# Kernel optimization log

Measured on AMD Instinct MI355X. Metric: run time of the kernel, lower is better.

The kernel has to match this reference:

```python
import jax, jax.numpy as jnp
import numpy as np

B, N, D, H = 32, 64, 128, 256
LN_EPS = 1e-5


def _mlp(x, W1, b1, g, beta, W2, b2):
    # Linear -> LayerNorm -> GELU (exact erf) -> Linear
    h = x @ W1 + b1
    mu = jnp.mean(h, axis=-1, keepdims=True)
    var = jnp.var(h, axis=-1, keepdims=True)
    h = (h - mu) * jax.lax.rsqrt(var + LN_EPS) * g + beta
    h = jax.nn.gelu(h, approximate=False)
    return h @ W2 + b2


def setup_inputs() -> dict:
    key = jax.random.key(0)
    ks = jax.random.split(key, 10)
    s = lambda fan_in: 1.0 / np.sqrt(fan_in)
    return {
        "slots": jax.random.normal(ks[0], (B, N, D), dtype=jnp.float32),
        "adjacency": jax.random.uniform(ks[1], (B, N, N), dtype=jnp.float32),
        # edge_net params
        "We1": jax.random.uniform(ks[2], (2 * D, H), minval=-s(2 * D), maxval=s(2 * D), dtype=jnp.float32),
        "be1": jnp.zeros((H,), jnp.float32),
        "ge": jnp.ones((H,), jnp.float32),
        "bge": jnp.zeros((H,), jnp.float32),
        "We2": jax.random.uniform(ks[3], (H, D), minval=-s(H), maxval=s(H), dtype=jnp.float32),
        "be2": jnp.zeros((D,), jnp.float32),
        # node_net params
        "Wn1": jax.random.uniform(ks[4], (2 * D, H), minval=-s(2 * D), maxval=s(2 * D), dtype=jnp.float32),
        "bn1": jnp.zeros((H,), jnp.float32),
        "gn": jnp.ones((H,), jnp.float32),
        "bgn": jnp.zeros((H,), jnp.float32),
        "Wn2": jax.random.uniform(ks[5], (H, D), minval=-s(H), maxval=s(H), dtype=jnp.float32),
        "bn2": jnp.zeros((D,), jnp.float32),
    }


def reference(slots, adjacency, We1, be1, ge, bge, We2, be2, Wn1, bn1, gn, bgn, Wn2, bn2):
    b, n, d = slots.shape
    # all-pairs edge features: receiver i, sender j -> [B,N,N,2D]
    ei = jnp.broadcast_to(slots[:, :, None, :], (b, n, n, d))
    ej = jnp.broadcast_to(slots[:, None, :, :], (b, n, n, d))
    edge_feat = jnp.concatenate([ei, ej], axis=-1)
    edge_out = _mlp(edge_feat, We1, be1, ge, bge, We2, be2)  # [B,N,N,D]
    # mask diagonal (i != j) and weight by adjacency, then reduce over j
    mask = 1.0 - jnp.eye(n, dtype=slots.dtype)
    w = adjacency * mask  # [B,N,N]
    messages = jnp.einsum('bij,bijd->bid', w, edge_out)
    node_input = jnp.concatenate([slots, messages], axis=-1)
    delta = _mlp(node_input, Wn1, bn1, gn, bgn, Wn2, bn2)
    return slots + delta
```

## Files before the change

kernel.cpp:

```cpp
#include <hip/hip_runtime.h>

#define NB 32
#define NN 64
#define ND 128
#define NH 256
#define LN_EPS 1e-5f
#define RP 4

__device__ __forceinline__ float gelu2(float x) {
    const float au  = fabsf(x);
    const float xpa = x + au;
    const float z   = au * 0.70710678118654752440f;
    const float z2  = z * z;
    const float pc  = fmaf(0.078108f, z, 0.000972f);
    const float pb  = fmaf(0.278393f, z, 1.0f);
    const float p   = fmaf(z2, fmaf(z, pc, 0.230389f), pb);
    const float p2  = p * p;
    const float r   = __builtin_amdgcn_rcpf(p2 * p2);
    return fmaf(-au, r, xpa);
}
__device__ __forceinline__ float gelu_h(float x) { return 0.5f * gelu2(x); }

__global__ __launch_bounds__(256) void k_pre(const float* __restrict__ slots,
                                             const float* __restrict__ We1,
                                             const float* __restrict__ be1,
                                             const float* __restrict__ Wn1,
                                             const float* __restrict__ We2,
                                             const float* __restrict__ be2,
                                             float* __restrict__ Pt,
                                             float* __restrict__ Qm,
                                             float* __restrict__ XW,
                                             float4* __restrict__ rowstats,
                                             float* __restrict__ WC,
                                             float* __restrict__ v) {
    __shared__ float xs[RP][ND];
    __shared__ float red[4][RP][4];
    const int t = threadIdx.x;

    if (blockIdx.x >= 512) {
        const int bid2 = blockIdx.x - 512;
        if (bid2 == 64) {
            __shared__ float bs[ND];
            if (t < ND) bs[t] = be2[t];
            __syncthreads();
            float acc = 0.f;
            #pragma unroll 4
            for (int d = 0; d < ND; ++d) acc = fmaf(bs[d], Wn1[(ND + d) * NH + t], acc);
            v[t] = acc;
            return;
        }
        const int k0 = bid2 * 4;
        __shared__ float ws[4][ND];
        #pragma unroll
        for (int i = 0; i < 2; ++i) {
            const int idx = t + i * 256;
            ws[idx >> 7][idx & 127] = We2[(k0 + (idx >> 7)) * ND + (idx & 127)];
        }
        __syncthreads();
        float acc[4] = {0.f, 0.f, 0.f, 0.f};
        #pragma unroll 4
        for (int d = 0; d < ND; ++d) {
            const float wn = Wn1[(ND + d) * NH + t];
            #pragma unroll
            for (int r = 0; r < 4; ++r) acc[r] = fmaf(ws[r][d], wn, acc[r]);
        }
        #pragma unroll
        for (int r = 0; r < 4; ++r) WC[(k0 + r) * NH + t] = acc[r];
        return;
    }

    const int r0 = blockIdx.x * RP;
    const int lane = t & 63, wave = t >> 6;
    #pragma unroll
    for (int i = 0; i < 2; ++i) {
        const int idx = t + i * 256;
        xs[idx >> 7][idx & 127] = slots[(size_t)(r0 + (idx >> 7)) * ND + (idx & 127)];
    }
    __syncthreads();
    float pt[RP], qq[RP], xw[RP];
    const float bb = be1[t];
    #pragma unroll
    for (int r = 0; r < RP; ++r) { pt[r] = bb; qq[r] = 0.f; xw[r] = 0.f; }
    #pragma unroll 4
    for (int d = 0; d < ND; ++d) {
        const float wt  = We1[d * NH + t];
        const float wbt = We1[(ND + d) * NH + t];
        const float wn  = Wn1[d * NH + t];
        #pragma unroll
        for (int r = 0; r < RP; ++r) {
            const float x = xs[r][d];
            pt[r] = fmaf(x, wt,  pt[r]);
            qq[r] = fmaf(x, wbt, qq[r]);
            xw[r] = fmaf(x, wn,  xw[r]);
        }
    }
    #pragma unroll
    for (int r = 0; r < RP; ++r) {
        const size_t row = (size_t)(r0 + r);
        Pt[row * NH + t] = pt[r];
        Qm[row * NH + t] = qq[r];
        XW[row * NH + t] = xw[r];
    }
    float s1[RP], s2[RP], s3[RP], s4[RP];
    #pragma unroll
    for (int r = 0; r < RP; ++r) {
        s1[r] = pt[r]; s2[r] = pt[r] * pt[r];
        s3[r] = qq[r]; s4[r] = qq[r] * qq[r];
    }
    #pragma unroll
    for (int off = 32; off; off >>= 1) {
        #pragma unroll
        for (int r = 0; r < RP; ++r) {
            s1[r] += __shfl_xor(s1[r], off);
            s2[r] += __shfl_xor(s2[r], off);
            s3[r] += __shfl_xor(s3[r], off);
            s4[r] += __shfl_xor(s4[r], off);
        }
    }
    if (lane == 0) {
        #pragma unroll
        for (int r = 0; r < RP; ++r) {
            red[wave][r][0] = s1[r]; red[wave][r][1] = s2[r];
            red[wave][r][2] = s3[r]; red[wave][r][3] = s4[r];
        }
    }
    __syncthreads();
    if (t < RP) {
        float4 st;
        st.x = (red[0][t][0] + red[1][t][0]) + (red[2][t][0] + red[3][t][0]);
        st.y = (red[0][t][1] + red[1][t][1]) + (red[2][t][1] + red[3][t][1]);
        st.z = (red[0][t][2] + red[1][t][2]) + (red[2][t][2] + red[3][t][2]);
        st.w = (red[0][t][3] + red[1][t][3]) + (red[2][t][3] + red[3][t][3]);
        rowstats[r0 + t] = st;
    }
}

__global__ __launch_bounds__(256, 8) void k_mn(
    const float* __restrict__ slots,
    const float* __restrict__ adj,
    const float* __restrict__ Pt,
    const float* __restrict__ Qm,
    const float4* __restrict__ rowstats,
    const float* __restrict__ ge,  const float* __restrict__ bge,
    const float* __restrict__ XW,
    const float* __restrict__ WC, const float* __restrict__ v,
    const float* __restrict__ bn1,
    const float* __restrict__ gn,  const float* __restrict__ bgn,
    const float* __restrict__ Wn2, const float* __restrict__ bn2,
    float* __restrict__ out)
{
    union U {
        struct { float pt[2][NH]; float4 wmr[2][NN]; float s[4][2][NH]; } b;
        struct { float sf[2][NH]; float g[2][NH];    float d[2][8][ND]; } c;
    };
    __shared__ U u;
    __shared__ float lds_ws[2];
    __shared__ float lds_red[4][2][2];
    __shared__ float lds_mr[2][2];

    const int bid  = blockIdx.x;
    const int row0 = bid * 2;
    const int b    = row0 >> 6;
    const int i0   = row0 & 63;
    const int t    = threadIdx.x;
    const int lane = t & 63;
    const int wave = t >> 6;

    u.b.pt[0][t] = Pt[(size_t)row0 * NH + t];
    u.b.pt[1][t] = Pt[(size_t)(row0 + 1) * NH + t];
    __syncthreads();

    const int jp = t >> 2, part = t & 3;
    {
        float cd0 = 0.f, cd1 = 0.f;
        const float4* qrow = (const float4*)(Qm + ((size_t)b * NN + jp) * NH) + part * 16;
        const float4* p0   = (const float4*)u.b.pt[0] + part * 16;
        const float4* p1   = (const float4*)u.b.pt[1] + part * 16;
        #pragma unroll 4
        for (int k = 0; k < 16; ++k) {
            const float4 q = qrow[k];
            const float4 a = p0[k];
            const float4 c = p1[k];
            cd0 = fmaf(a.x, q.x, fmaf(a.y, q.y, fmaf(a.z, q.z, fmaf(a.w, q.w, cd0))));
            cd1 = fmaf(c.x, q.x, fmaf(c.y, q.y, fmaf(c.z, q.z, fmaf(c.w, q.w, cd1))));
        }
        cd0 += __shfl_xor(cd0, 1); cd0 += __shfl_xor(cd0, 2);
        cd1 += __shfl_xor(cd1, 1); cd1 += __shfl_xor(cd1, 2);
        if (part == 0) {
            const float inv = 1.0f / NH;
            const float4 stj = rowstats[(size_t)b * NN + jp];
            const float4 st0 = rowstats[row0];
            const float4 st1 = rowstats[row0 + 1];
            float a0 = adj[(size_t)row0 * NN + jp];       if (jp == i0)     a0 = 0.f;
            float a1 = adj[(size_t)(row0 + 1) * NN + jp]; if (jp == i0 + 1) a1 = 0.f;
            {
                const float mu = (st0.x + stj.z) * inv;
                const float e2 = fmaf(2.f, cd0, st0.y + stj.w) * inv;
                const float rr = __builtin_amdgcn_rsqf(fmaf(-mu, mu, e2) + LN_EPS);
                u.b.wmr[0][jp] = make_float4(0.5f * a0, rr, -mu * rr, a0);
            }
            {
                const float mu = (st1.x + stj.z) * inv;
                const float e2 = fmaf(2.f, cd1, st1.y + stj.w) * inv;
                const float rr = __builtin_amdgcn_rsqf(fmaf(-mu, mu, e2) + LN_EPS);
                u.b.wmr[1][jp] = make_float4(0.5f * a1, rr, -mu * rr, a1);
            }
        }
    }
    __syncthreads();

    if (wave < 2) {
        float wv = u.b.wmr[wave][lane].w;
        #pragma unroll
        for (int off = 32; off; off >>= 1) wv += __shfl_xor(wv, off);
        if (lane == 0) lds_ws[wave] = wv;
    }

    const float4 P0 = ((const float4*)u.b.pt[0])[lane];
    const float4 P1 = ((const float4*)u.b.pt[1])[lane];
    const float4 G  = ((const float4*)ge)[lane];
    const float4 Bg = ((const float4*)bge)[lane];
    const float4* Qb = (const float4*)(Qm + (size_t)b * NN * NH) + lane;
    float4 A0 = make_float4(0.f, 0.f, 0.f, 0.f);
    float4 A1 = make_float4(0.f, 0.f, 0.f, 0.f);
    #pragma unroll 4
    for (int k = 0; k < 16; ++k) {
        const int jj = wave + 4 * k;
        const float4 q  = Qb[jj * (NH / 4)];
        const float4 m0 = u.b.wmr[0][jj];
        const float4 m1 = u.b.wmr[1][jj];
        float h, uu;
        h = P0.x + q.x; uu = fmaf(fmaf(h, m0.y, m0.z), G.x, Bg.x); A0.x = fmaf(m0.x, gelu2(uu), A0.x);
        h = P0.y + q.y; uu = fmaf(fmaf(h, m0.y, m0.z), G.y, Bg.y); A0.y = fmaf(m0.x, gelu2(uu), A0.y);
        h = P0.z + q.z; uu = fmaf(fmaf(h, m0.y, m0.z), G.z, Bg.z); A0.z = fmaf(m0.x, gelu2(uu), A0.z);
        h = P0.w + q.w; uu = fmaf(fmaf(h, m0.y, m0.z), G.w, Bg.w); A0.w = fmaf(m0.x, gelu2(uu), A0.w);
        h = P1.x + q.x; uu = fmaf(fmaf(h, m1.y, m1.z), G.x, Bg.x); A1.x = fmaf(m1.x, gelu2(uu), A1.x);
        h = P1.y + q.y; uu = fmaf(fmaf(h, m1.y, m1.z), G.y, Bg.y); A1.y = fmaf(m1.x, gelu2(uu), A1.y);
        h = P1.z + q.z; uu = fmaf(fmaf(h, m1.y, m1.z), G.z, Bg.z); A1.z = fmaf(m1.x, gelu2(uu), A1.z);
        h = P1.w + q.w; uu = fmaf(fmaf(h, m1.y, m1.z), G.w, Bg.w); A1.w = fmaf(m1.x, gelu2(uu), A1.w);
    }
    ((float4*)u.b.s[wave][0])[lane] = A0;
    ((float4*)u.b.s[wave][1])[lane] = A1;
    __syncthreads();

    const float sf0 = (u.b.s[0][0][t] + u.b.s[1][0][t]) + (u.b.s[2][0][t] + u.b.s[3][0][t]);
    const float sf1 = (u.b.s[0][1][t] + u.b.s[1][1][t]) + (u.b.s[2][1][t] + u.b.s[3][1][t]);
    __syncthreads();
    u.c.sf[0][t] = sf0;
    u.c.sf[1][t] = sf1;
    __syncthreads();

    float a0, a1;
    {
        const float b1 = bn1[t], vc = v[t];
        a0 = fmaf(lds_ws[0], vc, b1) + XW[(size_t)row0 * NH + t];
        a1 = fmaf(lds_ws[1], vc, b1) + XW[(size_t)(row0 + 1) * NH + t];
        const float* wc = WC + t;
        #pragma unroll 8
        for (int k = 0; k < NH; ++k) {
            const float w = wc[k * NH];
            a0 = fmaf(u.c.sf[0][k], w, a0);
            a1 = fmaf(u.c.sf[1][k], w, a1);
        }
    }
    {
        float s1 = a0, s2 = a0 * a0, s3 = a1, s4 = a1 * a1;
        #pragma unroll
        for (int off = 32; off; off >>= 1) {
            s1 += __shfl_xor(s1, off); s2 += __shfl_xor(s2, off);
            s3 += __shfl_xor(s3, off); s4 += __shfl_xor(s4, off);
        }
        if (lane == 0) {
            lds_red[wave][0][0] = s1; lds_red[wave][0][1] = s2;
            lds_red[wave][1][0] = s3; lds_red[wave][1][1] = s4;
        }
    }
    __syncthreads();
    if (t < 2) {
        const float S1 = (lds_red[0][t][0] + lds_red[1][t][0]) + (lds_red[2][t][0] + lds_red[3][t][0]);
        const float S2 = (lds_red[0][t][1] + lds_red[1][t][1]) + (lds_red[2][t][1] + lds_red[3][t][1]);
        const float mu  = S1 * (1.0f / NH);
        const float var = fmaf(-mu, mu, S2 * (1.0f / NH));
        lds_mr[t][0] = mu;
        lds_mr[t][1] = __builtin_amdgcn_rsqf(var + LN_EPS);
    }
    __syncthreads();
    {
        const float g = gn[t], bg = bgn[t];
        const float rr0 = lds_mr[0][1], rr1 = lds_mr[1][1];
        u.c.g[0][t] = gelu_h(fmaf(fmaf(a0, rr0, -lds_mr[0][0] * rr0), g, bg));
        u.c.g[1][t] = gelu_h(fmaf(fmaf(a1, rr1, -lds_mr[1][0] * rr1), g, bg));
    }
    __syncthreads();

    {
        const int ks = t >> 5;
        const int cg = t & 31;
        float4 d0 = make_float4(0.f, 0.f, 0.f, 0.f);
        float4 d1 = make_float4(0.f, 0.f, 0.f, 0.f);
        const float4* w2 = (const float4*)Wn2 + cg;
        const int kbeg = ks * 32;
        #pragma unroll 8
        for (int k = kbeg; k < kbeg + 32; ++k) {
            const float4 w = w2[k * (ND / 4)];
            const float g0 = u.c.g[0][k];
            const float g1 = u.c.g[1][k];
            d0.x = fmaf(g0, w.x, d0.x); d0.y = fmaf(g0, w.y, d0.y);
            d0.z = fmaf(g0, w.z, d0.z); d0.w = fmaf(g0, w.w, d0.w);
            d1.x = fmaf(g1, w.x, d1.x); d1.y = fmaf(g1, w.y, d1.y);
            d1.z = fmaf(g1, w.z, d1.z); d1.w = fmaf(g1, w.w, d1.w);
        }
        ((float4*)u.c.d[0][ks])[cg] = d0;
        ((float4*)u.c.d[1][ks])[cg] = d1;
    }
    __syncthreads();
    {
        const int r  = t >> 7;
        const int c2 = t & 127;
        float ds = 0.f;
        #pragma unroll
        for (int p2 = 0; p2 < 8; ++p2) ds += u.c.d[r][p2][c2];
        const size_t o = (size_t)(row0 + r) * ND + c2;
        out[o] = slots[o] + bn2[c2] + ds;
    }
}

extern "C" void kernel_launch(void* const* d_in, const int* in_sizes, int n_in,
                              void* d_out, int out_size, void* d_ws, size_t ws_size,
                              hipStream_t stream) {
    const float* slots = (const float*)d_in[0];
    const float* adj   = (const float*)d_in[1];
    const float* We1   = (const float*)d_in[2];
    const float* be1   = (const float*)d_in[3];
    const float* ge    = (const float*)d_in[4];
    const float* bge   = (const float*)d_in[5];
    const float* We2   = (const float*)d_in[6];
    const float* be2   = (const float*)d_in[7];
    const float* Wn1   = (const float*)d_in[8];
    const float* bn1   = (const float*)d_in[9];
    const float* gn    = (const float*)d_in[10];
    const float* bgn   = (const float*)d_in[11];
    const float* Wn2   = (const float*)d_in[12];
    const float* bn2   = (const float*)d_in[13];
    float* out = (float*)d_out;

    const size_t RN = (size_t)NB * NN;
    float*  Ptw   = (float*)d_ws;
    float*  Qw    = Ptw   + RN * NH;
    float*  XWw   = Qw    + RN * NH;
    float*  WCw   = XWw   + RN * NH;
    float*  vw    = WCw   + (size_t)NH * NH;
    float4* rsw   = (float4*)(vw + NH);

    k_pre<<<577,       256, 0, stream>>>(slots, We1, be1, Wn1, We2, be2,
                                         Ptw, Qw, XWw, rsw, WCw, vw);
    k_mn <<<(int)(RN / 2), 256, 0, stream>>>(slots, adj, Ptw, Qw, rsw, ge, bge,
                                             XWw, WCw, vw, bn1, gn, bgn, Wn2, bn2, out);
}
```

Baseline: 61.52 us.

## Move pairwise LayerNorm dot products to a bf16 MFMA kernel

Adds a separate k_dot kernel that computes all P·Q row dot products per batch with bf16 MFMA 16x16x32 and writes the per-edge LN scale, shift and adjacency weights to a global workspace. k_pre also emits bf16 copies of P and Q for it. k_mn drops its inline fp32 dot-product phase and instead loads the precomputed table. It also splits the WC matvec across waves with an LDS partial reduction and lowers the occupancy hint. This adds a third launch, extra global traffic, and bf16 rounding in the variance term, which may hurt accuracy through cancellation.

```diff
diff --git a/kernel.cpp b/kernel.cpp
--- a/kernel.cpp
+++ b/kernel.cpp
@@ -6,6 +6,9 @@
 #define NH 256
 #define LN_EPS 1e-5f
 #define RP 4
+
+typedef __attribute__((ext_vector_type(8))) short bf16x8;
+typedef __attribute__((ext_vector_type(4))) float f32x4;
 
 __device__ __forceinline__ float gelu2(float x) {
     const float au  = fabsf(x);
@@ -21,6 +24,12 @@
 }
 __device__ __forceinline__ float gelu_h(float x) { return 0.5f * gelu2(x); }
 
+__device__ __forceinline__ short f2bf(float f) {
+    unsigned u = __float_as_uint(f);
+    u += 0x7FFFu + ((u >> 16) & 1u);
+    return (short)(u >> 16);
+}
+
 __global__ __launch_bounds__(256) void k_pre(const float* __restrict__ slots,
                                              const float* __restrict__ We1,
                                              const float* __restrict__ be1,
@@ -30,6 +39,8 @@
                                              float* __restrict__ Pt,
                                              float* __restrict__ Qm,
                                              float* __restrict__ XW,
+                                             short* __restrict__ Pb,
+                                             short* __restrict__ Qb,
                                              float4* __restrict__ rowstats,
                                              float* __restrict__ WC,
                                              float* __restrict__ v) {
@@ -100,6 +111,8 @@
         Pt[row * NH + t] = pt[r];
         Qm[row * NH + t] = qq[r];
         XW[row * NH + t] = xw[r];
+        Pb[row * NH + t] = f2bf(pt[r]);
+        Qb[row * NH + t] = f2bf(qq[r]);
     }
     float s1[RP], s2[RP], s3[RP], s4[RP];
     #pragma unroll
@@ -135,12 +148,54 @@
     }
 }
 
-__global__ __launch_bounds__(256, 8) void k_mn(
+__global__ __launch_bounds__(256) void k_dot(
+    const short* __restrict__ Pb, const short* __restrict__ Qb,
+    const float4* __restrict__ rowstats,
+    const float* __restrict__ adj,
+    float4* __restrict__ wmrG)
+{
+    const int b  = blockIdx.x >> 2;
+    const int jt = blockIdx.x & 3;
+    const int t  = threadIdx.x;
+    const int l  = t & 63;
+    const int i0 = (t >> 6) * 16;
+    const int j0 = jt * 16;
+    const int rA = l & 15;
+    const int kg = l >> 4;
+
+    const short* Prow = Pb + ((size_t)b * NN + i0 + rA) * NH + kg * 8;
+    const short* Qrow = Qb + ((size_t)b * NN + j0 + rA) * NH + kg * 8;
+    f32x4 acc = {0.f, 0.f, 0.f, 0.f};
+    #pragma unroll
+    for (int kc = 0; kc < 8; ++kc) {
+        const bf16x8 av = *(const bf16x8*)(Prow + kc * 32);
+        const bf16x8 bv = *(const bf16x8*)(Qrow + kc * 32);
+        acc = __builtin_amdgcn_mfma_f32_16x16x32_bf16(av, bv, acc, 0, 0, 0);
+    }
+    const int j  = j0 + (l & 15);
+    const int gj = b * NN + j;
+    const float4 stj = rowstats[gj];
+    const float inv = 1.0f / NH;
+    #pragma unroll
+    for (int q = 0; q < 4; ++q) {
+        const int i  = i0 + (l >> 4) * 4 + q;
+        const int gi = b * NN + i;
+        const float4 sti = rowstats[gi];
+        float a = adj[(size_t)gi * NN + j];
+        if (j == i) a = 0.f;
+        const float cd = acc[q];
+        const float mu = (sti.x + stj.z) * inv;
+        const float e2 = fmaf(2.f, cd, sti.y + stj.w) * inv;
+        const float rr = __builtin_amdgcn_rsqf(fmaf(-mu, mu, e2) + LN_EPS);
+        wmrG[(size_t)gi * NN + j] = make_float4(0.5f * a, rr, -mu * rr, a);
+    }
+}
+
+__global__ __launch_bounds__(256, 4) void k_mn(
     const float* __restrict__ slots,
-    const float* __restrict__ adj,
     const float* __restrict__ Pt,
     const float* __restrict__ Qm,
-    const float4* __restrict__ rowstats,
+    const float4* __restrict__ wmrG,
     const float* __restrict__ ge,  const float* __restrict__ bge,
     const float* __restrict__ XW,
     const float* __restrict__ WC, const float* __restrict__ v,
@@ -150,85 +205,50 @@
     float* __restrict__ out)
 {
     union U {
-        struct { float pt[2][NH]; float4 wmr[2][NN]; float s[4][2][NH]; } b;
-        struct { float sf[2][NH]; float g[2][NH];    float d[2][8][ND]; } c;
+        struct { float4 wmr[2][NN]; float s[4][2][NH]; } e;
+        struct { float sfg[2][NH];
+                 union { float part[2][4][NH]; float d[2][8][ND + 4]; } w; } n;
     };
     __shared__ U u;
     __shared__ float lds_ws[2];
     __shared__ float lds_red[4][2][2];
     __shared__ float lds_mr[2][2];
 
-    const int bid  = blockIdx.x;
-    const int row0 = bid * 2;
+    const int row0 = blockIdx.x * 2;
     const int b    = row0 >> 6;
-    const int i0   = row0 & 63;
     const int t    = threadIdx.x;
     const int lane = t & 63;
     const int wave = t >> 6;
 
-    u.b.pt[0][t] = Pt[(size_t)row0 * NH + t];
-    u.b.pt[1][t] = Pt[(size_t)(row0 + 1) * NH + t];
-    __syncthreads();
-
-    const int jp = t >> 2, part = t & 3;
-    {
-        float cd0 = 0.f, cd1 = 0.f;
-        const float4* qrow = (const float4*)(Qm + ((size_t)b * NN + jp) * NH) + part * 16;
-        const float4* p0   = (const float4*)u.b.pt[0] + part * 16;
-        const float4* p1   = (const float4*)u.b.pt[1] + part * 16;
-        #pragma unroll 4
-        for (int k = 0; k < 16; ++k) {
-            const float4 q = qrow[k];
-            const float4 a = p0[k];
-            const float4 c = p1[k];
-            cd0 = fmaf(a.x, q.x, fmaf(a.y, q.y, fmaf(a.z, q.z, fmaf(a.w, q.w, cd0))));
-            cd1 = fmaf(c.x, q.x, fmaf(c.y, q.y, fmaf(c.z, q.z, fmaf(c.w, q.w, cd1))));
-        }
-        cd0 += __shfl_xor(cd0, 1); cd0 += __shfl_xor(cd0, 2);
-        cd1 += __shfl_xor(cd1, 1); cd1 += __shfl_xor(cd1, 2);
-        if (part == 0) {
-            const float inv = 1.0f / NH;
-            const float4 stj = rowstats[(size_t)b * NN + jp];
-            const float4 st0 = rowstats[row0];
-            const float4 st1 = rowstats[row0 + 1];
-            float a0 = adj[(size_t)row0 * NN + jp];       if (jp == i0)     a0 = 0.f;
-            float a1 = adj[(size_t)(row0 + 1) * NN + jp]; if (jp == i0 + 1) a1 = 0.f;
-            {
-                const float mu = (st0.x + stj.z) * inv;
-                const float e2 = fmaf(2.f, cd0, st0.y + stj.w) * inv;
-                const float rr = __builtin_amdgcn_rsqf(fmaf(-mu, mu, e2) + LN_EPS);
-                u.b.wmr[0][jp] = make_float4(0.5f * a0, rr, -mu * rr, a0);
-            }
-            {
-                const float mu = (st1.x + stj.z) * inv;
-                const float e2 = fmaf(2.f, cd1, st1.y + stj.w) * inv;
-                const float rr = __builtin_amdgcn_rsqf(fmaf(-mu, mu, e2) + LN_EPS);
-                u.b.wmr[1][jp] = make_float4(0.5f * a1, rr, -mu * rr, a1);
-            }
-        }
-    }
+    const float xw0 = XW[(size_t)row0 * NH + t];
+    const float xw1 = XW[(size_t)(row0 + 1) * NH + t];
+    const float sl  = slots[(size_t)(row0 + (t >> 7)) * ND + (t & 127)];
+    if (t < 128) {
+        const int r = t >> 6, j = t & 63;
+        u.e.wmr[r][j] = wmrG[(size_t)(row0 + r) * NN + j];
+    }
+    const float4 P0 = ((const float4*)(Pt + (size_t)row0 * NH))[lane];
+    const float4 P1 = ((const float4*)(Pt + (size_t)(row0 + 1) * NH))[lane];
+    const float4 G  = ((const float4*)ge)[lane];
+    const float4 Bg = ((const float4*)bge)[lane];
     __syncthreads();
 
     if (wave < 2) {
-        float wv = u.b.wmr[wave][lane].w;
+        float wv = u.e.wmr[wave][lane].w;
         #pragma unroll
         for (int off = 32; off; off >>= 1) wv += __shfl_xor(wv, off);
         if (lane == 0) lds_ws[wave] = wv;
     }
 
-    const float4 P0 = ((const float4*)u.b.pt[0])[lane];
-    const float4 P1 = ((const float4*)u.b.pt[1])[lane];
-    const float4 G  = ((const float4*)ge)[lane];
-    const float4 Bg = ((const float4*)bge)[lane];
-    const float4* Qb = (const float4*)(Qm + (size_t)b * NN * NH) + lane;
+    const float4* Qb4 = (const float4*)(Qm + (size_t)b * NN * NH) + lane;
     float4 A0 = make_float4(0.f, 0.f, 0.f, 0.f);
     float4 A1 = make_float4(0.f, 0.f, 0.f, 0.f);
     #pragma unroll 4
     for (int k = 0; k < 16; ++k) {
         const int jj = wave + 4 * k;
-        const float4 q  = Qb[jj * (NH / 4)];
-        const float4 m0 = u.b.wmr[0][jj];
-        const float4 m1 = u.b.wmr[1][jj];
+        const float4 q  = Qb4[jj * (NH / 4)];
+        const float4 m0 = u.e.wmr[0][jj];
+        const float4 m1 = u.e.wmr[1][jj];
         float h, uu;
         h = P0.x + q.x; uu = fmaf(fmaf(h, m0.y, m0.z), G.x, Bg.x); A0.x = fmaf(m0.x, gelu2(uu), A0.x);
         h = P0.y + q.y; uu = fmaf(fmaf(h, m0.y, m0.z), G.y, Bg.y); A0.y = fmaf(m0.x, gelu2(uu), A0.y);
@@ -239,29 +259,46 @@
         h = P1.z + q.z; uu = fmaf(fmaf(h, m1.y, m1.z), G.z, Bg.z); A1.z = fmaf(m1.x, gelu2(uu), A1.z);
         h = P1.w + q.w; uu = fmaf(fmaf(h, m1.y, m1.z), G.w, Bg.w); A1.w = fmaf(m1.x, gelu2(uu), A1.w);
     }
-    ((float4*)u.b.s[wave][0])[lane] = A0;
-    ((float4*)u.b.s[wave][1])[lane] = A1;
-    __syncthreads();
-
-    const float sf0 = (u.b.s[0][0][t] + u.b.s[1][0][t]) + (u.b.s[2][0][t] + u.b.s[3][0][t]);
-    const float sf1 = (u.b.s[0][1][t] + u.b.s[1][1][t]) + (u.b.s[2][1][t] + u.b.s[3][1][t]);
-    __syncthreads();
-    u.c.sf[0][t] = sf0;
-    u.c.sf[1][t] = sf1;
+    ((float4*)u.e.s[wave][0])[lane] = A0;
+    ((float4*)u.e.s[wave][1])[lane] = A1;
+    __syncthreads();
+
+    const float sf0 = (u.e.s[0][0][t] + u.e.s[1][0][t]) + (u.e.s[2][0][t] + u.e.s[3][0][t]);
+    const float sf1 = (u.e.s[0][1][t] + u.e.s[1][1][t]) + (u.e.s[2][1][t] + u.e.s[3][1][t]);
+    u.n.sfg[0][t] = sf0;
+    u.n.sfg[1][t] = sf1;
+    __syncthreads();
+
+    {
+        const int ks = wave;
+        const int cg = lane;
+        float4 h0 = make_float4(0.f, 0.f, 0.f, 0.f);
+        float4 h1 = make_float4(0.f, 0.f, 0.f, 0.f);
+        const float4* wc4 = (const float4*)WC + cg;
+        #pragma unroll 8
+        for (int k = ks * 64; k < ks * 64 + 64; ++k) {
+            const float4 w = wc4[k * (NH / 4)];
+            const float sa = u.n.sfg[0][k];
+            const float sb = u.n.sfg[1][k];
+            h0.x = fmaf(sa, w.x, h0.x); h0.y = fmaf(sa, w.y, h0.y);
+            h0.z = fmaf(sa, w.z, h0.z); h0.w = fmaf(sa, w.w, h0.w);
+            h1.x = fmaf(sb, w.x, h1.x); h1.y = fmaf(sb, w.y, h1.y);
+            h1.z = fmaf(sb, w.z, h1.z); h1.w = fmaf(sb, w.w, h1.w);
+        }
+        ((float4*)u.n.w.part[0][ks])[cg] = h0;
+        ((float4*)u.n.w.part[1][ks])[cg] = h1;
+    }
     __syncthreads();
 
     float a0, a1;
     {
         const float b1 = bn1[t], vc = v[t];
-        a0 = fmaf(lds_ws[0], vc, b1) + XW[(size_t)row0 * NH + t];
-        a1 = fmaf(lds_ws[1], vc, b1) + XW[(size_t)(row0 + 1) * NH + t];
-        const float* wc = WC + t;
-        #pragma unroll 8
-        for (int k = 0; k < NH; ++k) {
-            const float w = wc[k * NH];
-            a0 = fmaf(u.c.sf[0][k], w, a0);
-            a1 = fmaf(u.c.sf[1][k], w, a1);
-        }
+        a0 = (u.n.w.part[0][0][t] + u.n.w.part[0][1][t])
+           + (u.n.w.part[0][2][t] + u.n.w.part[0][3][t])
+           + fmaf(lds_ws[0], vc, b1) + xw0;
+        a1 = (u.n.w.part[1][0][t] + u.n.w.part[1][1][t])
+           + (u.n.w.part[1][2][t] + u.n.w.part[1][3][t])
+           + fmaf(lds_ws[1], vc, b1) + xw1;
     }
     {
         float s1 = a0, s2 = a0 * a0, s3 = a1, s4 = a1 * a1;
@@ -288,8 +325,8 @@
     {
         const float g = gn[t], bg = bgn[t];
         const float rr0 = lds_mr[0][1], rr1 = lds_mr[1][1];
-        u.c.g[0][t] = gelu_h(fmaf(fmaf(a0, rr0, -lds_mr[0][0] * rr0), g, bg));
-        u.c.g[1][t] = gelu_h(fmaf(fmaf(a1, rr1, -lds_mr[1][0] * rr1), g, bg));
+        u.n.sfg[0][t] = gelu_h(fmaf(fmaf(a0, rr0, -lds_mr[0][0] * rr0), g, bg));
+        u.n.sfg[1][t] = gelu_h(fmaf(fmaf(a1, rr1, -lds_mr[1][0] * rr1), g, bg));
     }
     __syncthreads();
 
@@ -303,15 +340,15 @@
         #pragma unroll 8
         for (int k = kbeg; k < kbeg + 32; ++k) {
             const float4 w = w2[k * (ND / 4)];
-            const float g0 = u.c.g[0][k];
-            const float g1 = u.c.g[1][k];
+            const float g0 = u.n.sfg[0][k];
+            const float g1 = u.n.sfg[1][k];
             d0.x = fmaf(g0, w.x, d0.x); d0.y = fmaf(g0, w.y, d0.y);
             d0.z = fmaf(g0, w.z, d0.z); d0.w = fmaf(g0, w.w, d0.w);
             d1.x = fmaf(g1, w.x, d1.x); d1.y = fmaf(g1, w.y, d1.y);
             d1.z = fmaf(g1, w.z, d1.z); d1.w = fmaf(g1, w.w, d1.w);
         }
-        ((float4*)u.c.d[0][ks])[cg] = d0;
-        ((float4*)u.c.d[1][ks])[cg] = d1;
+        ((float4*)u.n.w.d[0][ks])[cg] = d0;
+        ((float4*)u.n.w.d[1][ks])[cg] = d1;
     }
     __syncthreads();
     {
@@ -319,9 +356,8 @@
         const int c2 = t & 127;
         float ds = 0.f;
         #pragma unroll
-        for (int p2 = 0; p2 < 8; ++p2) ds += u.c.d[r][p2][c2];
-        const size_t o = (size_t)(row0 + r) * ND + c2;
-        out[o] = slots[o] + bn2[c2] + ds;
+        for (int p2 = 0; p2 < 8; ++p2) ds += u.n.w.d[r][p2][c2];
+        out[(size_t)(row0 + r) * ND + c2] = sl + bn2[c2] + ds;
     }
 }
 
@@ -345,15 +381,19 @@
     float* out = (float*)d_out;
 
     const size_t RN = (size_t)NB * NN;
-    float*  Ptw   = (float*)d_ws;
-    float*  Qw    = Ptw   + RN * NH;
-    float*  XWw   = Qw    + RN * NH;
-    float*  WCw   = XWw   + RN * NH;
-    float*  vw    = WCw   + (size_t)NH * NH;
-    float4* rsw   = (float4*)(vw + NH);
-
-    k_pre<<<577,       256, 0, stream>>>(slots, We1, be1, Wn1, We2, be2,
-                                         Ptw, Qw, XWw, rsw, WCw, vw);
-    k_mn <<<(int)(RN / 2), 256, 0, stream>>>(slots, adj, Ptw, Qw, rsw, ge, bge,
+    float*  Ptw  = (float*)d_ws;
+    float*  Qw   = Ptw  + RN * NH;
+    float*  XWw  = Qw   + RN * NH;
+    float*  WCw  = XWw  + RN * NH;
+    float*  vw   = WCw  + (size_t)NH * NH;
+    float4* rsw  = (float4*)(vw + NH);
+    float4* wmrw = rsw + RN;
+    short*  Pbw  = (short*)(wmrw + RN * NN);
+    short*  Qbw  = Pbw + RN * NH;
+
+    k_pre<<<577,           256, 0, stream>>>(slots, We1, be1, Wn1, We2, be2,
+                                             Ptw, Qw, XWw, Pbw, Qbw, rsw, WCw, vw);
+    k_dot<<<NB * 4,        256, 0, stream>>>(Pbw, Qbw, rsw, adj, wmrw);
+    k_mn <<<(int)(RN / 2), 256, 0, stream>>>(slots, Ptw, Qw, wmrw, ge, bge,
                                              XWw, WCw, vw, bn1, gn, bgn, Wn2, bn2, out);
 }
```

Result: faster. 56.98 us (-7.4%).
